# Kernel tuning notes

Measured on AMD Instinct MI355X. Metric: run time of the kernel, lower is better.

Reference implementation:

```python
import jax, jax.numpy as jnp
import numpy as np

N = 500_000   # num nodes
F = 128       # num_features
H = 128       # hidden
B = 32_768    # batch size
K = 4         # hops
RWS = 16      # random walks per batch node
E = RWS * B   # sampled edges per hop
ALPHA = 0.1
OUT = 8


def setup_inputs() -> dict:
    key = jax.random.key(0)
    ks = jax.random.split(key, 12)
    x = jax.random.normal(ks[0], (N, F), dtype=jnp.float32)
    degree = jax.random.uniform(ks[1], (N,), dtype=jnp.float32, minval=1.0, maxval=64.0)
    batch = jax.random.randint(ks[2], (B,), 0, N, dtype=jnp.int32)
    heads_idx = jax.random.randint(ks[3], (K, E), 0, B, dtype=jnp.int32)
    ends = jax.random.randint(ks[4], (K, E), 0, N, dtype=jnp.int32)
    # MLP params (Kaiming-ish scaling)
    W0 = jax.random.normal(ks[5], (F, H), dtype=jnp.float32) / np.float32(np.sqrt(F))
    b0 = jnp.zeros((H,), dtype=jnp.float32)
    W1 = jax.random.normal(ks[6], (H, H), dtype=jnp.float32) / np.float32(np.sqrt(H))
    b1 = jnp.zeros((H,), dtype=jnp.float32)
    W2 = jax.random.normal(ks[7], (H, OUT), dtype=jnp.float32) / np.float32(np.sqrt(H))
    b2 = jnp.zeros((OUT,), dtype=jnp.float32)
    # APPNP attention weights: alpha*(1-alpha)^k, last = (1-alpha)^K
    att = np.float32(ALPHA) * np.float32(1.0 - ALPHA) ** np.arange(K + 1, dtype=np.float32)
    att[-1] = np.float32(1.0 - ALPHA) ** np.float32(K)
    att = jnp.asarray(att)
    return {"x": x, "W0": W0, "b0": b0, "W1": W1, "b1": b1, "W2": W2, "b2": b2,
            "att": att, "degree": degree, "batch": batch,
            "heads_idx": heads_idx, "ends": ends}


def reference(x, W0, b0, W1, b1, W2, b2, att, degree, batch, heads_idx, ends):
    # eval mode: dropout is a no-op
    dis = degree ** -0.5  # deg_inv_sqrt

    def mlp(feats):  # lins[1](relu(lins[0](feats)))
        h = jax.nn.relu(feats @ W0 + b0)
        return h @ W1 + b1

    nb = batch.shape[0]
    ne = jnp.float32(ends.shape[1])
    dsum = degree[batch].sum()

    aggx = att[0] * mlp(x[batch])                       # [B, H]
    for k in range(K):  # small fixed hop count
        heads = heads_idx[k]                            # local rows in [0, B)
        e = ends[k]                                     # global node ids
        val = dis[batch[heads]] * dis[e] * (dsum / ne)  # [E]
        tmp = mlp(x[e]) * val[:, None]                  # gather + MLP + weight
        aggx = aggx + att[k + 1] * jax.ops.segment_sum(tmp, heads, num_segments=nb)
    out = jax.nn.relu(aggx) @ W2 + b2                   # [B, 8]
    return jax.nn.log_softmax(out, axis=1)
```

## Files before the change

### kernel.cpp

```cpp
#include <hip/hip_runtime.h>

#define NN 500000
#define FF 128
#define HH 128
#define BB 32768
#define KHOPS 4
#define EPER 524288
#define KE (KHOPS * EPER)
#define NOUT 8
#define SBLK 256
#define EPB (KE / SBLK)
#define GEMM_TILES 3907

typedef unsigned short u16;
typedef unsigned char u8;
typedef __attribute__((ext_vector_type(8))) short short8v;
typedef __attribute__((ext_vector_type(4))) float f32x4;
typedef __attribute__((ext_vector_type(2))) float f32x2;

__device__ __forceinline__ float bflo(unsigned int u) {
    union { unsigned int x; float f; } t; t.x = u << 16; return t.f;
}
__device__ __forceinline__ float bfhi(unsigned int u) {
    union { unsigned int x; float f; } t; t.x = u & 0xFFFF0000u; return t.f;
}
__device__ __forceinline__ u16 f2bf(float f) {
    union { float f; unsigned int u; } t; t.f = f;
    unsigned int u = t.u;
    unsigned int r = (u + 0x7FFFu + ((u >> 16) & 1u)) >> 16;
    return (u16)r;
}

__launch_bounds__(256, 2)
__global__ void k_pre1(const int* __restrict__ heads, u8* __restrict__ M,
                       const float* __restrict__ deg, const int* __restrict__ batch,
                       float* __restrict__ dsum, const float* __restrict__ W0,
                       u16* __restrict__ w0p, float* __restrict__ dis) {
    __shared__ unsigned int hp[8192];
    int tid = threadIdx.x;
    int bid = blockIdx.x;
    if (bid < SBLK) {
        #pragma unroll
        for (int j = 0; j < 32; j++) hp[tid + j * 256] = 0;
        __syncthreads();
        int ebase = bid * EPB;
        #pragma unroll 4
        for (int it = 0; it < EPB / 256; it++) {
            int b = heads[ebase + it * 256 + tid];
            atomicAdd(&hp[b >> 2], 1u << ((b & 3) * 8));
        }
        __syncthreads();
        unsigned int* M32 = (unsigned int*)(M + (size_t)bid * BB);
        #pragma unroll
        for (int j = 0; j < 32; j++) {
            int w = tid + j * 256;
            M32[w] = hp[w];
        }
    } else if (bid == SBLK) {
        float* red = (float*)hp;
        float a0 = 0.f, a1 = 0.f, a2 = 0.f, a3 = 0.f;
        for (int i = tid; i < BB; i += 1024) {
            a0 += deg[batch[i]];
            a1 += deg[batch[i + 256]];
            a2 += deg[batch[i + 512]];
            a3 += deg[batch[i + 768]];
        }
        red[tid] = (a0 + a1) + (a2 + a3);
        __syncthreads();
        for (int off = 128; off > 0; off >>= 1) {
            if (tid < off) red[tid] += red[tid + off];
            __syncthreads();
        }
        if (tid == 0) dsum[0] = red[0];
    } else if (bid == SBLK + 1) {
        for (int r = 0; r < 64; r++) {
            int f = r * 256 + tid;
            int k = f >> 7, c = f & 127;
            int kt = k >> 5, i = k & 7, lh = (k >> 3) & 3;
            int lane = lh * 16 + (c & 15), n = c >> 4;
            w0p[(((kt * 8 + n) * 64 + lane) << 3) + i] = f2bf(W0[f]);
        }
    } else {
        int i0 = (bid - SBLK - 2) * 1024 + tid * 4;
        if (i0 < NN) {
            float4 d = *(const float4*)&deg[i0];
            float4 o;
            o.x = rsqrtf(d.x); o.y = rsqrtf(d.y);
            o.z = rsqrtf(d.z); o.w = rsqrtf(d.w);
            *(float4*)&dis[i0] = o;
        }
    }
}

__global__ void k_pre2(u8* __restrict__ M, int* __restrict__ colsum,
                       const float* __restrict__ deg, const int* __restrict__ batch,
                       const float* __restrict__ dsum, float* __restrict__ disb) {
    int tid = threadIdx.x;
    if (blockIdx.x < 32) {
        int g = blockIdx.x * 256 + tid;
        unsigned int* M32 = (unsigned int*)M;
        unsigned int run = 0;
        #pragma unroll 8
        for (int b = 0; b < SBLK; b++) {
            size_t idx = (size_t)b * (BB / 4) + g;
            unsigned int v = M32[idx];
            M32[idx] = run;
            run += v;
        }
        colsum[g * 4 + 0] = (int)(run & 0xFFu);
        colsum[g * 4 + 1] = (int)((run >> 8) & 0xFFu);
        colsum[g * 4 + 2] = (int)((run >> 16) & 0xFFu);
        colsum[g * 4 + 3] = (int)((run >> 24) & 0xFFu);
    } else {
        int b0 = (blockIdx.x - 32) * 1024 + tid * 4;
        float sc = dsum[0] * (1.0f / (float)EPER);
        #pragma unroll
        for (int t = 0; t < 4; t++) {
            int b = b0 + t;
            disb[b] = rsqrtf(deg[batch[b]]) * sc;
        }
    }
}

__global__ void k_scan(const int* __restrict__ colsum, int* __restrict__ base) {
    __shared__ int sc[1024];
    int tid = threadIdx.x;
    int loc[32];
    int run = 0;
    #pragma unroll
    for (int j = 0; j < 32; j++) {
        loc[j] = run;
        run += colsum[tid * 32 + j];
    }
    sc[tid] = run;
    __syncthreads();
    for (int off = 1; off < 1024; off <<= 1) {
        int v = (tid >= off) ? sc[tid - off] : 0;
        __syncthreads();
        sc[tid] += v;
        __syncthreads();
    }
    int excl = sc[tid] - run;
    #pragma unroll
    for (int j = 0; j < 32; j++) base[tid * 32 + j] = excl + loc[j];
    if (tid == 1023) base[BB] = sc[1023];
}

__launch_bounds__(256, 2)
__global__ void k_scatter2(const int* __restrict__ heads, const int* __restrict__ ends,
                           const u8* __restrict__ M, const int* __restrict__ base,
                           const float* __restrict__ dis, const float* __restrict__ disb,
                           const float* __restrict__ att, uint2* __restrict__ ewp) {
    __shared__ unsigned int hp[8192];
    int tid = threadIdx.x, blk = blockIdx.x;
    float attk = att[(blk >> 6) + 1];
    #pragma unroll
    for (int j = 0; j < 32; j++) hp[tid + j * 256] = 0;
    __syncthreads();
    int ebase = blk * EPB;
    for (int it = 0; it < EPB / 256; it++) {
        int i = ebase + it * 256 + tid;
        int b = heads[i];
        int e = ends[i];
        float w = attk * disb[b] * dis[e];
        unsigned int old = atomicAdd(&hp[b >> 2], 1u << ((b & 3) * 8));
        unsigned int rank = (old >> ((b & 3) * 8)) & 0xFFu;
        int pos = base[b] + (int)M[(size_t)blk * BB + b] + (int)rank;
        uint2 pw;
        pw.x = (unsigned int)e;
        pw.y = __float_as_uint(w);
        ewp[pos] = pw;
    }
}

__launch_bounds__(256, 5)
__global__ void k_gemm1(const float* __restrict__ x, const u16* __restrict__ w0p,
                        const float* __restrict__ b0, u16* __restrict__ h) {
    __shared__ u16 xs[128 * 128];
    int tid = threadIdx.x;
    int wid = tid >> 6;
    int lane = tid & 63;
    long rowbase = (long)blockIdx.x * 128;

    #pragma unroll
    for (int r = 0; r < 16; r++) {
        int f = tid + r * 256;
        int row = f >> 5;
        int c4 = (f & 31) * 4;
        long grow = rowbase + row; if (grow >= NN) grow = NN - 1;
        float4 v = *(const float4*)&x[grow * 128 + c4];
        ushort4 pv;
        pv.x = f2bf(v.x); pv.y = f2bf(v.y); pv.z = f2bf(v.z); pv.w = f2bf(v.w);
        int byte = row * 256 + ((c4 * 2) ^ ((row & 7) << 4));
        *(ushort4*)((char*)xs + byte) = pv;
    }
    __syncthreads();

    short8v a[2][4];
    #pragma unroll
    for (int rs = 0; rs < 2; rs++) {
        int row = wid * 32 + rs * 16 + (lane & 15);
        int sw = (row & 7) << 4;
        #pragma unroll
        for (int kt = 0; kt < 4; kt++) {
            int kb = kt * 64 + (lane >> 4) * 16;
            a[rs][kt] = *(const short8v*)((const char*)xs + row * 256 + (kb ^ sw));
        }
    }

    f32x4 acc[2][8] = {};
    #pragma unroll
    for (int n = 0; n < 8; n++) {
        short8v bfr[4];
        #pragma unroll
        for (int kt = 0; kt < 4; kt++)
            bfr[kt] = *(const short8v*)&w0p[(((kt * 8 + n) * 64 + lane) << 3)];
        #pragma unroll
        for (int rs = 0; rs < 2; rs++) {
            #pragma unroll
            for (int kt = 0; kt < 4; kt++)
                acc[rs][n] = __builtin_amdgcn_mfma_f32_16x16x32_bf16(
                                 a[rs][kt], bfr[kt], acc[rs][n], 0, 0, 0);
        }
    }

    float b0v[8];
    #pragma unroll
    for (int n = 0; n < 8; n++) b0v[n] = b0[n * 16 + (lane & 15)];

    u16* xw = &xs[wid * 32 * 128];
    #pragma unroll
    for (int rs = 0; rs < 2; rs++) {
        #pragma unroll
        for (int r = 0; r < 4; r++) {
            int row = rs * 16 + (lane >> 4) * 4 + r;
            int sw = (row & 7) << 4;
            #pragma unroll
            for (int n = 0; n < 8; n++) {
                float v = acc[rs][n][r] + b0v[n];
                v = v > 0.f ? v : 0.f;
                int byte = row * 256 + ((n * 32 + (lane & 15) * 2) ^ sw);
                *(u16*)((char*)xw + byte) = f2bf(v);
            }
        }
    }
    __syncthreads();
    #pragma unroll
    for (int pass = 0; pass < 8; pass++) {
        int off = pass * 1024 + lane * 16;
        int row = off >> 8;
        int colb = off & 255;
        int ocolb = colb ^ ((row & 7) << 4);
        long grow = rowbase + wid * 32 + row;
        uint4 v = *(const uint4*)((const char*)xw + off);
        if (grow < NN)
            *(uint4*)((char*)&h[grow * 128] + ocolb) = v;
    }
}

__launch_bounds__(256)
__global__ void k_gather(const u16* __restrict__ h, const int* __restrict__ batch,
                         const int* __restrict__ base, const uint2* __restrict__ ewp,
                         const float* __restrict__ att,
                         float* __restrict__ P, float* __restrict__ s) {
    int b = blockIdx.x * 4 + (threadIdx.x >> 6);
    int l = threadIdx.x & 63;
    int q = l >> 4;
    int c8 = (l & 15) * 8;
    float att0 = att[0];
    f32x2 acc2[4] = {{0.f, 0.f}, {0.f, 0.f}, {0.f, 0.f}, {0.f, 0.f}};
    float wsum = 0.f;

    if (q == 0) {
        int nb = batch[b];
        uint4 v = *(const uint4*)&h[(size_t)nb * 128 + c8];
        acc2[0] = f32x2{att0 * bflo(v.x), att0 * bfhi(v.x)};
        acc2[1] = f32x2{att0 * bflo(v.y), att0 * bfhi(v.y)};
        acc2[2] = f32x2{att0 * bflo(v.z), att0 * bfhi(v.z)};
        acc2[3] = f32x2{att0 * bflo(v.w), att0 * bfhi(v.w)};
    }

    int beg = base[b], fin = base[b + 1];
    for (int j = beg; j < fin; j += 32) {
        uint2 pw[8];
        #pragma unroll
        for (int u = 0; u < 8; u++) {
            int je = j + u * 4 + q;
            int jc = je < fin ? je : beg;
            pw[u] = ewp[jc];
            if (je >= fin) pw[u].y = 0u;
        }
        uint4 v[8];
        #pragma unroll
        for (int u = 0; u < 8; u++)
            v[u] = *(const uint4*)&h[(size_t)pw[u].x * 128 + c8];
        #pragma unroll
        for (int u = 0; u < 8; u++) {
            float w = __uint_as_float(pw[u].y);
            f32x2 w2 = {w, w};
            acc2[0] = __builtin_elementwise_fma(w2, f32x2{bflo(v[u].x), bfhi(v[u].x)}, acc2[0]);
            acc2[1] = __builtin_elementwise_fma(w2, f32x2{bflo(v[u].y), bfhi(v[u].y)}, acc2[1]);
            acc2[2] = __builtin_elementwise_fma(w2, f32x2{bflo(v[u].z), bfhi(v[u].z)}, acc2[2]);
            acc2[3] = __builtin_elementwise_fma(w2, f32x2{bflo(v[u].w), bfhi(v[u].w)}, acc2[3]);
            wsum += w;
        }
    }
    float accf[8] = { acc2[0].x, acc2[0].y, acc2[1].x, acc2[1].y,
                      acc2[2].x, acc2[2].y, acc2[3].x, acc2[3].y };
    #pragma unroll
    for (int k = 0; k < 8; k++) {
        accf[k] += __shfl_xor(accf[k], 16);
        accf[k] += __shfl_xor(accf[k], 32);
    }
    wsum += __shfl_xor(wsum, 16);
    wsum += __shfl_xor(wsum, 32);

    if (q == 0) {
        float4 o0 = { accf[0], accf[1], accf[2], accf[3] };
        float4 o1 = { accf[4], accf[5], accf[6], accf[7] };
        *(float4*)&P[(size_t)b * 128 + c8]     = o0;
        *(float4*)&P[(size_t)b * 128 + c8 + 4] = o1;
        if (l == 0) s[b] = att0 + wsum;
    }
}

__launch_bounds__(256, 2)
__global__ void k_out(const float* __restrict__ P, const float* __restrict__ s,
                      const float* __restrict__ W1, const float* __restrict__ b1,
                      const float* __restrict__ W2, const float* __restrict__ b2,
                      float* __restrict__ out) {
    __shared__ float W1s[128 * 128];
    __shared__ float Ps[32 * 128];
    int tid = threadIdx.x;
    int rowbase = blockIdx.x * 32;
    #pragma unroll
    for (int rep = 0; rep < 16; rep++) {
        int f = tid + rep * 256;
        *(float4*)&W1s[f * 4] = *(const float4*)&W1[f * 4];
    }
    #pragma unroll
    for (int rep = 0; rep < 4; rep++) {
        int f = tid + rep * 256;
        *(float4*)&Ps[f * 4] = *(const float4*)&P[(size_t)rowbase * 128 + f * 4];
    }
    __syncthreads();

    int c0 = (tid & 31) * 4;
    int r0 = (tid >> 5) * 4;
    float b1r[4] = { b1[c0], b1[c0 + 1], b1[c0 + 2], b1[c0 + 3] };
    float sv[4];
    #pragma unroll
    for (int j = 0; j < 4; j++) sv[j] = s[rowbase + r0 + j];

    float acc[4][4] = {};
    #pragma unroll 2
    for (int i = 0; i < 128; i += 4) {
        float4 xq[4], wq4[4];
        #pragma unroll
        for (int j = 0; j < 4; j++) xq[j]  = *(const float4*)&Ps[(r0 + j) * 128 + i];
        #pragma unroll
        for (int q = 0; q < 4; q++) wq4[q] = *(const float4*)&W1s[(i + q) * 128 + c0];
        #pragma unroll
        for (int j = 0; j < 4; j++) {
            float xv[4] = { xq[j].x, xq[j].y, xq[j].z, xq[j].w };
            #pragma unroll
            for (int q = 0; q < 4; q++) {
                acc[j][0] += xv[q] * wq4[q].x;
                acc[j][1] += xv[q] * wq4[q].y;
                acc[j][2] += xv[q] * wq4[q].z;
                acc[j][3] += xv[q] * wq4[q].w;
            }
        }
    }
    __syncthreads();
    #pragma unroll
    for (int j = 0; j < 4; j++) {
        #pragma unroll
        for (int c = 0; c < 4; c++) {
            float v = acc[j][c] + sv[j] * b1r[c];
            Ps[(r0 + j) * 128 + c0 + c] = v > 0.f ? v : 0.f;
        }
    }
    __syncthreads();

    int row = tid >> 3;
    int o = tid & 7;
    int rot = (row * 4) & 127;
    float v = b2[o];
    #pragma unroll 4
    for (int ii = 0; ii < 128; ii++) {
        int i = (ii + rot) & 127;
        v += Ps[row * 128 + i] * W2[i * 8 + o];
    }
    float m = v;
    for (int d = 1; d < 8; d <<= 1) m = fmaxf(m, __shfl_xor(m, d, 8));
    float ex = expf(v - m);
    float sum = ex;
    for (int d = 1; d < 8; d <<= 1) sum += __shfl_xor(sum, d, 8);
    out[(size_t)(rowbase + row) * 8 + o] = (v - m) - logf(sum);
}

extern "C" void kernel_launch(void* const* d_in, const int* in_sizes, int n_in,
                              void* d_out, int out_size, void* d_ws, size_t ws_size,
                              hipStream_t stream) {
    const float* x     = (const float*)d_in[0];
    const float* W0    = (const float*)d_in[1];
    const float* b0    = (const float*)d_in[2];
    const float* W1    = (const float*)d_in[3];
    const float* b1    = (const float*)d_in[4];
    const float* W2    = (const float*)d_in[5];
    const float* b2    = (const float*)d_in[6];
    const float* att   = (const float*)d_in[7];
    const float* deg   = (const float*)d_in[8];
    const int*   batch = (const int*)d_in[9];
    const int*   heads = (const int*)d_in[10];
    const int*   ends  = (const int*)d_in[11];
    float* out = (float*)d_out;

    char* w = (char*)d_ws;
    size_t off = 0;
    u16* h = (u16*)(w + off);          off += (size_t)NN * 128 * 2;
    float* P = (float*)(w + off);      off += (size_t)BB * 128 * 4;
    float* s = (float*)(w + off);      off += (size_t)BB * 4;
    int* base = (int*)(w + off);       off += 131328;
    uint2* ewp = (uint2*)(w + off);    off += (size_t)KE * 8;
    u8* M = (u8*)(w + off);            off += (size_t)SBLK * BB;
    int* colsum = (int*)(w + off);     off += (size_t)BB * 4;
    float* dis = (float*)(w + off);    off += (size_t)NN * 4;
    float* disb = (float*)(w + off);   off += (size_t)BB * 4;
    float* dsum = (float*)(w + off);   off += 256;
    u16* w0p = (u16*)(w + off);        off += 16384 * 2;

    int disBlocks = (NN + 1023) / 1024;
    k_pre1<<<SBLK + 2 + disBlocks, 256, 0, stream>>>(heads, M, deg, batch,
                                                     dsum, W0, w0p, dis);
    k_pre2<<<64, 256, 0, stream>>>(M, colsum, deg, batch, dsum, disb);
    k_scan<<<1, 1024, 0, stream>>>(colsum, base);
    k_scatter2<<<SBLK, 256, 0, stream>>>(heads, ends, M, base, dis, disb, att, ewp);
    k_gemm1<<<GEMM_TILES, 256, 0, stream>>>(x, w0p, b0, h);
    k_gather<<<BB / 4, 256, 0, stream>>>(h, batch, base, ewp, att, P, s);
    k_out<<<BB / 32, 256, 0, stream>>>(P, s, W1, b1, W2, b2, out);
}
```

Baseline: 370.9 us.

## Pack edge entries into 32-bit words and recompute weights in gather; shrink GEMM tile

The scatter kernel now writes a packed 32-bit word per edge (hop index in bits 19-20, node id in the low 19 bits) instead of an 8-byte (id, weight) pair, which halves the edge-list write and read traffic. The gather kernel recomputes each weight from att, disb and a dis[e] lookup, adding a dependent random load per edge. Separately, the first GEMM uses 64-row tiles with one 16-row slice per wave and launch bounds of 4, trading per-block reuse of W0 for more blocks and lower register pressure. The gather accumulators switch from packed f32x2 FMAs to scalar floats.

```diff
diff --git a/kernel.cpp b/kernel.cpp
--- a/kernel.cpp
+++ b/kernel.cpp
@@ -10,13 +10,12 @@
 #define NOUT 8
 #define SBLK 256
 #define EPB (KE / SBLK)
-#define GEMM_TILES 3907
+#define GEMM_TILES ((NN + 63) / 64)
 
 typedef unsigned short u16;
 typedef unsigned char u8;
 typedef __attribute__((ext_vector_type(8))) short short8v;
 typedef __attribute__((ext_vector_type(4))) float f32x4;
-typedef __attribute__((ext_vector_type(2))) float f32x2;
 
 __device__ __forceinline__ float bflo(unsigned int u) {
     union { unsigned int x; float f; } t; t.x = u << 16; return t.f;
@@ -149,11 +148,9 @@
 __launch_bounds__(256, 2)
 __global__ void k_scatter2(const int* __restrict__ heads, const int* __restrict__ ends,
                            const u8* __restrict__ M, const int* __restrict__ base,
-                           const float* __restrict__ dis, const float* __restrict__ disb,
-                           const float* __restrict__ att, uint2* __restrict__ ewp) {
+                           unsigned int* __restrict__ pe) {
     __shared__ unsigned int hp[8192];
     int tid = threadIdx.x, blk = blockIdx.x;
-    float attk = att[(blk >> 6) + 1];
     #pragma unroll
     for (int j = 0; j < 32; j++) hp[tid + j * 256] = 0;
     __syncthreads();
@@ -161,29 +158,26 @@
     for (int it = 0; it < EPB / 256; it++) {
         int i = ebase + it * 256 + tid;
         int b = heads[i];
-        int e = ends[i];
-        float w = attk * disb[b] * dis[e];
+        unsigned int e = (unsigned int)ends[i];
+        unsigned int kk = (unsigned int)(i >> 19);
         unsigned int old = atomicAdd(&hp[b >> 2], 1u << ((b & 3) * 8));
         unsigned int rank = (old >> ((b & 3) * 8)) & 0xFFu;
         int pos = base[b] + (int)M[(size_t)blk * BB + b] + (int)rank;
-        uint2 pw;
-        pw.x = (unsigned int)e;
-        pw.y = __float_as_uint(w);
-        ewp[pos] = pw;
-    }
-}
-
-__launch_bounds__(256, 5)
+        pe[pos] = (kk << 19) | e;
+    }
+}
+
+__launch_bounds__(256, 4)
 __global__ void k_gemm1(const float* __restrict__ x, const u16* __restrict__ w0p,
                         const float* __restrict__ b0, u16* __restrict__ h) {
-    __shared__ u16 xs[128 * 128];
+    __shared__ u16 xs[64 * 128];
     int tid = threadIdx.x;
     int wid = tid >> 6;
     int lane = tid & 63;
-    long rowbase = (long)blockIdx.x * 128;
-
-    #pragma unroll
-    for (int r = 0; r < 16; r++) {
+    long rowbase = (long)blockIdx.x * 64;
+
+    #pragma unroll
+    for (int r = 0; r < 8; r++) {
         int f = tid + r * 256;
         int row = f >> 5;
         int c4 = (f & 31) * 4;
@@ -196,19 +190,18 @@
     }
     __syncthreads();
 
-    short8v a[2][4];
-    #pragma unroll
-    for (int rs = 0; rs < 2; rs++) {
-        int row = wid * 32 + rs * 16 + (lane & 15);
+    short8v a[4];
+    {
+        int row = wid * 16 + (lane & 15);
         int sw = (row & 7) << 4;
         #pragma unroll
         for (int kt = 0; kt < 4; kt++) {
             int kb = kt * 64 + (lane >> 4) * 16;
-            a[rs][kt] = *(const short8v*)((const char*)xs + row * 256 + (kb ^ sw));
-        }
-    }
-
-    f32x4 acc[2][8] = {};
+            a[kt] = *(const short8v*)((const char*)xs + row * 256 + (kb ^ sw));
+        }
+    }
+
+    f32x4 acc[8] = {};
     #pragma unroll
     for (int n = 0; n < 8; n++) {
         short8v bfr[4];
@@ -216,42 +209,37 @@
         for (int kt = 0; kt < 4; kt++)
             bfr[kt] = *(const short8v*)&w0p[(((kt * 8 + n) * 64 + lane) << 3)];
         #pragma unroll
-        for (int rs = 0; rs < 2; rs++) {
-            #pragma unroll
-            for (int kt = 0; kt < 4; kt++)
-                acc[rs][n] = __builtin_amdgcn_mfma_f32_16x16x32_bf16(
-                                 a[rs][kt], bfr[kt], acc[rs][n], 0, 0, 0);
-        }
+        for (int kt = 0; kt < 4; kt++)
+            acc[n] = __builtin_amdgcn_mfma_f32_16x16x32_bf16(a[kt], bfr[kt],
+                                                             acc[n], 0, 0, 0);
     }
 
     float b0v[8];
     #pragma unroll
     for (int n = 0; n < 8; n++) b0v[n] = b0[n * 16 + (lane & 15)];
 
-    u16* xw = &xs[wid * 32 * 128];
-    #pragma unroll
-    for (int rs = 0; rs < 2; rs++) {
-        #pragma unroll
-        for (int r = 0; r < 4; r++) {
-            int row = rs * 16 + (lane >> 4) * 4 + r;
-            int sw = (row & 7) << 4;
-            #pragma unroll
-            for (int n = 0; n < 8; n++) {
-                float v = acc[rs][n][r] + b0v[n];
-                v = v > 0.f ? v : 0.f;
-                int byte = row * 256 + ((n * 32 + (lane & 15) * 2) ^ sw);
-                *(u16*)((char*)xw + byte) = f2bf(v);
-            }
-        }
-    }
-    __syncthreads();
-    #pragma unroll
-    for (int pass = 0; pass < 8; pass++) {
+    __syncthreads();
+    u16* xw = &xs[wid * 16 * 128];
+    #pragma unroll
+    for (int r = 0; r < 4; r++) {
+        int row = (lane >> 4) * 4 + r;
+        int sw = (row & 7) << 4;
+        #pragma unroll
+        for (int n = 0; n < 8; n++) {
+            float v = acc[n][r] + b0v[n];
+            v = v > 0.f ? v : 0.f;
+            int byte = row * 256 + ((n * 32 + (lane & 15) * 2) ^ sw);
+            *(u16*)((char*)xw + byte) = f2bf(v);
+        }
+    }
+    __syncthreads();
+    #pragma unroll
+    for (int pass = 0; pass < 4; pass++) {
         int off = pass * 1024 + lane * 16;
         int row = off >> 8;
         int colb = off & 255;
         int ocolb = colb ^ ((row & 7) << 4);
-        long grow = rowbase + wid * 32 + row;
+        long grow = rowbase + wid * 16 + row;
         uint4 v = *(const uint4*)((const char*)xw + off);
         if (grow < NN)
             *(uint4*)((char*)&h[grow * 128] + ocolb) = v;
@@ -260,7 +248,8 @@
 
 __launch_bounds__(256)
 __global__ void k_gather(const u16* __restrict__ h, const int* __restrict__ batch,
-                         const int* __restrict__ base, const uint2* __restrict__ ewp,
+                         const int* __restrict__ base, const unsigned int* __restrict__ pe,
+                         const float* __restrict__ dis, const float* __restrict__ disb,
                          const float* __restrict__ att,
                          float* __restrict__ P, float* __restrict__ s) {
     int b = blockIdx.x * 4 + (threadIdx.x >> 6);
@@ -268,56 +257,62 @@
     int q = l >> 4;
     int c8 = (l & 15) * 8;
     float att0 = att[0];
-    f32x2 acc2[4] = {{0.f, 0.f}, {0.f, 0.f}, {0.f, 0.f}, {0.f, 0.f}};
-    float wsum = 0.f;
+    float a1 = att[1], a2 = att[2], a3 = att[3], a4 = att[4];
+    float dbv = disb[b];
+    float acc[8] = {0.f, 0.f, 0.f, 0.f, 0.f, 0.f, 0.f, 0.f};
 
     if (q == 0) {
         int nb = batch[b];
         uint4 v = *(const uint4*)&h[(size_t)nb * 128 + c8];
-        acc2[0] = f32x2{att0 * bflo(v.x), att0 * bfhi(v.x)};
-        acc2[1] = f32x2{att0 * bflo(v.y), att0 * bfhi(v.y)};
-        acc2[2] = f32x2{att0 * bflo(v.z), att0 * bfhi(v.z)};
-        acc2[3] = f32x2{att0 * bflo(v.w), att0 * bfhi(v.w)};
+        acc[0] = att0 * bflo(v.x); acc[1] = att0 * bfhi(v.x);
+        acc[2] = att0 * bflo(v.y); acc[3] = att0 * bfhi(v.y);
+        acc[4] = att0 * bflo(v.z); acc[5] = att0 * bfhi(v.z);
+        acc[6] = att0 * bflo(v.w); acc[7] = att0 * bfhi(v.w);
     }
 
     int beg = base[b], fin = base[b + 1];
+    float wsum = 0.f;
     for (int j = beg; j < fin; j += 32) {
-        uint2 pw[8];
+        unsigned int p[8];
         #pragma unroll
         for (int u = 0; u < 8; u++) {
             int je = j + u * 4 + q;
             int jc = je < fin ? je : beg;
-            pw[u] = ewp[jc];
-            if (je >= fin) pw[u].y = 0u;
-        }
+            p[u] = pe[jc];
+            if (je >= fin) p[u] |= 0x80000000u;
+        }
+        float wv[8];
         uint4 v[8];
         #pragma unroll
-        for (int u = 0; u < 8; u++)
-            v[u] = *(const uint4*)&h[(size_t)pw[u].x * 128 + c8];
-        #pragma unroll
         for (int u = 0; u < 8; u++) {
-            float w = __uint_as_float(pw[u].y);
-            f32x2 w2 = {w, w};
-            acc2[0] = __builtin_elementwise_fma(w2, f32x2{bflo(v[u].x), bfhi(v[u].x)}, acc2[0]);
-            acc2[1] = __builtin_elementwise_fma(w2, f32x2{bflo(v[u].y), bfhi(v[u].y)}, acc2[1]);
-            acc2[2] = __builtin_elementwise_fma(w2, f32x2{bflo(v[u].z), bfhi(v[u].z)}, acc2[2]);
-            acc2[3] = __builtin_elementwise_fma(w2, f32x2{bflo(v[u].w), bfhi(v[u].w)}, acc2[3]);
+            int e = (int)(p[u] & 0x7FFFFu);
+            int kk = (int)((p[u] >> 19) & 3u);
+            float av = (kk < 2) ? (kk == 0 ? a1 : a2) : (kk == 2 ? a3 : a4);
+            float w = av * dbv * dis[e];
+            wv[u] = (p[u] & 0x80000000u) ? 0.f : w;
+            v[u] = *(const uint4*)&h[(size_t)e * 128 + c8];
+        }
+        #pragma unroll
+        for (int u = 0; u < 8; u++) {
+            float w = wv[u];
+            acc[0] += w * bflo(v[u].x); acc[1] += w * bfhi(v[u].x);
+            acc[2] += w * bflo(v[u].y); acc[3] += w * bfhi(v[u].y);
+            acc[4] += w * bflo(v[u].z); acc[5] += w * bfhi(v[u].z);
+            acc[6] += w * bflo(v[u].w); acc[7] += w * bfhi(v[u].w);
             wsum += w;
         }
     }
-    float accf[8] = { acc2[0].x, acc2[0].y, acc2[1].x, acc2[1].y,
-                      acc2[2].x, acc2[2].y, acc2[3].x, acc2[3].y };
     #pragma unroll
     for (int k = 0; k < 8; k++) {
-        accf[k] += __shfl_xor(accf[k], 16);
-        accf[k] += __shfl_xor(accf[k], 32);
+        acc[k] += __shfl_xor(acc[k], 16);
+        acc[k] += __shfl_xor(acc[k], 32);
     }
     wsum += __shfl_xor(wsum, 16);
     wsum += __shfl_xor(wsum, 32);
 
     if (q == 0) {
-        float4 o0 = { accf[0], accf[1], accf[2], accf[3] };
-        float4 o1 = { accf[4], accf[5], accf[6], accf[7] };
+        float4 o0 = { acc[0], acc[1], acc[2], acc[3] };
+        float4 o1 = { acc[4], acc[5], acc[6], acc[7] };
         *(float4*)&P[(size_t)b * 128 + c8]     = o0;
         *(float4*)&P[(size_t)b * 128 + c8 + 4] = o1;
         if (l == 0) s[b] = att0 + wsum;
@@ -423,7 +418,7 @@
     float* P = (float*)(w + off);      off += (size_t)BB * 128 * 4;
     float* s = (float*)(w + off);      off += (size_t)BB * 4;
     int* base = (int*)(w + off);       off += 131328;
-    uint2* ewp = (uint2*)(w + off);    off += (size_t)KE * 8;
+    unsigned int* pe = (unsigned int*)(w + off); off += (size_t)KE * 4;
     u8* M = (u8*)(w + off);            off += (size_t)SBLK * BB;
     int* colsum = (int*)(w + off);     off += (size_t)BB * 4;
     float* dis = (float*)(w + off);    off += (size_t)NN * 4;
@@ -436,8 +431,8 @@
                                                      dsum, W0, w0p, dis);
     k_pre2<<<64, 256, 0, stream>>>(M, colsum, deg, batch, dsum, disb);
     k_scan<<<1, 1024, 0, stream>>>(colsum, base);
-    k_scatter2<<<SBLK, 256, 0, stream>>>(heads, ends, M, base, dis, disb, att, ewp);
+    k_scatter2<<<SBLK, 256, 0, stream>>>(heads, ends, M, base, pe);
     k_gemm1<<<GEMM_TILES, 256, 0, stream>>>(x, w0p, b0, h);
-    k_gather<<<BB / 4, 256, 0, stream>>>(h, batch, base, ewp, att, P, s);
+    k_gather<<<BB / 4, 256, 0, stream>>>(h, batch, base, pe, dis, disb, att, P, s);
     k_out<<<BB / 32, 256, 0, stream>>>(P, s, W1, b1, W2, b2, out);
 }
```

New measurement: 360.3 us. -2.8%, faster.
